# Kernel tuning notes

Hardware: AMD Instinct MI355X
Metric: run time of the kernel (lower is better)

Reference implementation:

```python
import jax, jax.numpy as jnp
import numpy as np

N = 50000      # total nodes across all graphs
E = 1600000    # edges
G = 500        # graphs in batch
F = 128        # input node features
K = 5          # Chebyshev order


def setup_inputs() -> dict:
    key = jax.random.key(0)
    ks = jax.random.split(key, 12)
    x = jax.random.normal(ks[0], (N, F), dtype=jnp.float32)
    edge_index = jax.random.randint(ks[1], (2, E), 0, N)
    edge_attr = jax.random.uniform(ks[2], (E,), dtype=jnp.float32)
    batch = jnp.sort(jax.random.randint(ks[3], (N,), 0, G))
    s = 0.05
    W1 = jax.random.normal(ks[4], (K, F, 64), dtype=jnp.float32) * s
    b1 = jnp.zeros((64,), jnp.float32)
    W2 = jax.random.normal(ks[5], (K, 64, 64), dtype=jnp.float32) * s
    b2 = jnp.zeros((64,), jnp.float32)
    W3 = jax.random.normal(ks[6], (K, 64, 128), dtype=jnp.float32) * s
    b3 = jnp.zeros((128,), jnp.float32)
    Wl = jax.random.normal(ks[7], (128, 2), dtype=jnp.float32) * s
    bl = jnp.zeros((2,), jnp.float32)
    return {"x": x, "edge_index": edge_index, "edge_attr": edge_attr,
            "batch": batch, "W1": W1, "b1": b1, "W2": W2, "b2": b2,
            "W3": W3, "b3": b3, "Wl": Wl, "bl": bl}


def _cheb_conv(x, src, dst, w, Wk, b):
    """PyG ChebConv with lambda_max=2, sym norm: Lhat = -D^-1/2 A D^-1/2
    (the +I diag of L cancels the -I of the rescale, so only off-diag edges).
    Chebyshev recursion: Tx0=x, Tx1=Lhat x, Tx_k = 2 Lhat Tx_{k-1} - Tx_{k-2}."""
    n = x.shape[0]

    def prop(h):  # sparse matvec: out[i] = sum_{e: dst=i} w_e * h[src_e]
        return jax.ops.segment_sum(w[:, None] * h[src], dst, num_segments=n)

    Tx0 = x
    out = Tx0 @ Wk[0]
    Tx1 = prop(Tx0)
    out = out + Tx1 @ Wk[1]
    for k in range(2, Wk.shape[0]):
        Tx2 = 2.0 * prop(Tx1) - Tx0
        out = out + Tx2 @ Wk[k]
        Tx0, Tx1 = Tx1, Tx2
    return out + b


def reference(x, edge_index, edge_attr, batch, W1, b1, W2, b2, W3, b3, Wl, bl):
    src, dst = edge_index[0], edge_index[1]
    # sym-normalized scaled Laplacian edge weights (off-diagonal part)
    deg = jax.ops.segment_sum(edge_attr, src, num_segments=N)
    deg_safe = jnp.where(deg > 0, deg, 1.0)
    dinv = jnp.where(deg > 0, deg_safe ** -0.5, 0.0)
    w = -dinv[src] * edge_attr * dinv[dst]

    h = jax.nn.relu(_cheb_conv(x, src, dst, w, W1, b1))
    # dropout is identity at inference (training=False)
    h = jax.nn.relu(_cheb_conv(h, src, dst, w, W2, b2))
    h = jax.nn.relu(_cheb_conv(h, src, dst, w, W3, b3))

    # global_mean_pool over batch vector
    cnt = jax.ops.segment_sum(jnp.ones((N,), h.dtype), batch, num_segments=G)
    pooled = jax.ops.segment_sum(h, batch, num_segments=G) / jnp.maximum(cnt, 1.0)[:, None]

    logits = pooled @ Wl + bl
    return jax.nn.log_softmax(logits, axis=1)
```

## Files before the change

### kernel.cpp

```cpp
#include <hip/hip_runtime.h>
#include <hip/hip_bf16.h>

#define NN 50000
#define EE 1600000
#define GG 500

#define HB 6250
#define GX1 196
#define GB1 (GX1 * 5)
#define CVB 240

typedef __bf16 bf16x8 __attribute__((ext_vector_type(8)));
typedef float  f32x4  __attribute__((ext_vector_type(4)));

__device__ __forceinline__ float b2f(ushort u) {
  return __uint_as_float(((unsigned)u) << 16);
}
__device__ __forceinline__ ushort f2b(float f) {
  unsigned u = __float_as_uint(f);
  unsigned r = (u + 0x7fff + ((u >> 16) & 1)) >> 16;
  return (ushort)r;
}
__device__ __forceinline__ float lo16(uint v) { return __uint_as_float(v << 16); }
__device__ __forceinline__ float hi16(uint v) { return __uint_as_float(v & 0xffff0000u); }


__global__ __launch_bounds__(256) void mega1(
    const int* __restrict__ src, const int* __restrict__ dst,
    const float* __restrict__ ea, float* __restrict__ deg,
    int* __restrict__ cnt, int* __restrict__ rank,
    const float* __restrict__ x, const float* __restrict__ W1,
    ushort* __restrict__ Acat,
    const float* __restrict__ W2, const float* __restrict__ W3,
    ushort* __restrict__ Wt2, ushort* __restrict__ Wt3)
{
  int b = blockIdx.x;
  if (b < HB) {
    int i = b * 256 + threadIdx.x;
    if (i < EE) {
      atomicAdd(&deg[src[i]], ea[i]);
      rank[i] = atomicAdd(&cnt[dst[i]], 1);
    }
    return;
  }
  b -= HB;
  if (b < GB1) {
    const int bx = b % GX1, by = b / GX1;
    const int lane = threadIdx.x & 63;
    const int wid  = threadIdx.x >> 6;
    const int rb = bx * 256;
    const int cb = by * 64;
    const int lr = lane & 15;
    const int lk = (lane >> 4) << 3;
    f32x4 acc[4][4] = {};
    for (int kc = 0; kc < 128; kc += 64) {
      bf16x8 bfrag[2][4];
      #pragma unroll
      for (int ks = 0; ks < 2; ++ks)
        #pragma unroll
        for (int nt = 0; nt < 4; ++nt) {
          int col = cb + nt * 16 + lr;
          int kk  = kc + ks * 32 + lk;
          const float* wp = &W1[((size_t)(col >> 6) * 128 + kk) * 64 + (col & 63)];
          union { bf16x8 v; ushort u[8]; } bu;
          #pragma unroll
          for (int t = 0; t < 8; ++t) bu.u[t] = f2b(wp[t * 64]);
          bfrag[ks][nt] = bu.v;
        }
      #pragma unroll
      for (int s = 0; s < 4; ++s) {
        const int row = rb + (wid * 4 + s) * 16 + lr;
        #pragma unroll
        for (int ks = 0; ks < 2; ++ks) {
          union { bf16x8 v; ushort u[8]; } au;
          if (row < NN) {
            const float* ap = &x[(size_t)row * 128 + kc + ks * 32 + lk];
            float4 f0 = *(const float4*)ap;
            float4 f1 = *(const float4*)(ap + 4);
            au.u[0] = f2b(f0.x); au.u[1] = f2b(f0.y);
            au.u[2] = f2b(f0.z); au.u[3] = f2b(f0.w);
            au.u[4] = f2b(f1.x); au.u[5] = f2b(f1.y);
            au.u[6] = f2b(f1.z); au.u[7] = f2b(f1.w);
          } else {
            au.v = bf16x8{};
          }
          #pragma unroll
          for (int nt = 0; nt < 4; ++nt)
            acc[s][nt] = __builtin_amdgcn_mfma_f32_16x16x32_bf16(au.v, bfrag[ks][nt],
                                                                 acc[s][nt], 0, 0, 0);
        }
      }
    }
    #pragma unroll
    for (int s = 0; s < 4; ++s)
      #pragma unroll
      for (int nt = 0; nt < 4; ++nt) {
        const int col = cb + nt * 16 + lr;
        #pragma unroll
        for (int r = 0; r < 4; ++r) {
          const int row = rb + (wid * 4 + s) * 16 + ((lane >> 4) << 2) + r;
          if (row < NN) Acat[(size_t)row * 320 + col] = f2b(acc[s][nt][r]);
        }
      }
    return;
  }
  b -= GB1;
  int t = b * 256 + threadIdx.x;
  if (t < 320 * 64) {
    int j = t / 64, k = t % 64;
    Wt2[t] = f2b(W2[((size_t)(j >> 6) * 64 + k) * 64 + (j & 63)]);
  } else {
    int t2 = t - 320 * 64;
    int j = t2 / 320, k = t2 % 320;
    Wt3[t2] = f2b(W3[(size_t)k * 128 + j]);
  }
}


__global__ void scan1(const int* __restrict__ cnt, float* __restrict__ deg,
                      int* __restrict__ partial, int* __restrict__ bsum, int n) {
  __shared__ int s[256];
  int t = threadIdx.x, i = blockIdx.x * 256 + t;
  if (i < n) { float d = deg[i]; deg[i] = (d > 0.f) ? (1.0f / sqrtf(d)) : 0.f; }
  int v = (i < n) ? ((cnt[i] + 7) & ~7) : 0;
  s[t] = v; __syncthreads();
  for (int off = 1; off < 256; off <<= 1) {
    int xv = (t >= off) ? s[t - off] : 0;
    __syncthreads(); s[t] += xv; __syncthreads();
  }
  if (i < n) partial[i] = s[t];
  if (t == 255) bsum[blockIdx.x] = s[255];
}

__global__ void scan2(int* __restrict__ bsum, int nb) {
  __shared__ int s[256];
  int t = threadIdx.x;
  int v = (t < nb) ? bsum[t] : 0;
  s[t] = v; __syncthreads();
  for (int off = 1; off < 256; off <<= 1) {
    int xv = (t >= off) ? s[t - off] : 0;
    __syncthreads(); s[t] += xv; __syncthreads();
  }
  if (t < nb) bsum[t] = s[t];
}

__global__ void scan3(const int* __restrict__ partial, const int* __restrict__ bsum,
                      const int* __restrict__ cnt, int* __restrict__ rowptr,
                      uint2* __restrict__ edges, int n) {
  int i = blockIdx.x * 256 + threadIdx.x;
  if (i < n) {
    int off = (blockIdx.x > 0) ? bsum[blockIdx.x - 1] : 0;
    int end = partial[i] + off;
    rowptr[i + 1] = end;
    if (i == 0) rowptr[0] = 0;
    int c = cnt[i];
    int start = end - ((c + 7) & ~7);
    for (int q = start + c; q < end; ++q) edges[q] = make_uint2(0u, 0u);
  }
}

__global__ void scatter_kernel(const int* __restrict__ src, const int* __restrict__ dst,
                               const float* __restrict__ ea, const float* __restrict__ dinv,
                               const int* __restrict__ rowptr, const int* __restrict__ rank,
                               uint2* __restrict__ edges, int e) {
  int i = blockIdx.x * blockDim.x + threadIdx.x;
  if (i < e) {
    int s = src[i], d = dst[i];
    float w = -dinv[s] * ea[i] * dinv[d];
    edges[rowptr[d] + rank[i]] = make_uint2((unsigned)s, __float_as_uint(w));
  }
}


template<int NADD, bool RELUB>
__global__ __launch_bounds__(256) void prop_kernel(
    const int* __restrict__ rowptr, const uint2* __restrict__ edges,
    const ushort* __restrict__ g, int sg,
    const ushort* __restrict__ a1, int sa1, float c1,
    const ushort* __restrict__ a2, int sa2, float c2,
    const float* __restrict__ bias,
    ushort* __restrict__ out, int so, int n, float alpha)
{
  int wv = blockIdx.x * 4 + (threadIdx.x >> 6);
  wv = __builtin_amdgcn_readfirstlane(wv);
  const int lane = threadIdx.x & 63;
  const int grp = lane >> 3;
  const int sub = lane & 7;
  if (wv >= n) return;
  const int e0 = __builtin_amdgcn_readfirstlane(rowptr[wv]);
  const int e1 = __builtin_amdgcn_readfirstlane(rowptr[wv + 1]);

  float ra[8] = {}, rb[8] = {};
  int j = e0;
  for (; j + 16 <= e1; j += 16) {
    uint2 pa = edges[j + grp];
    uint2 pb = edges[j + 8 + grp];
    uint4 va = *(const uint4*)&g[(size_t)pa.x * sg + sub * 8];
    uint4 vb = *(const uint4*)&g[(size_t)pb.x * sg + sub * 8];
    float wa = __uint_as_float(pa.y);
    float wb = __uint_as_float(pb.y);
    ra[0] += wa * lo16(va.x); ra[1] += wa * hi16(va.x);
    ra[2] += wa * lo16(va.y); ra[3] += wa * hi16(va.y);
    ra[4] += wa * lo16(va.z); ra[5] += wa * hi16(va.z);
    ra[6] += wa * lo16(va.w); ra[7] += wa * hi16(va.w);
    rb[0] += wb * lo16(vb.x); rb[1] += wb * hi16(vb.x);
    rb[2] += wb * lo16(vb.y); rb[3] += wb * hi16(vb.y);
    rb[4] += wb * lo16(vb.z); rb[5] += wb * hi16(vb.z);
    rb[6] += wb * lo16(vb.w); rb[7] += wb * hi16(vb.w);
  }
  if (j < e1) {
    uint2 p = edges[j + grp];
    uint4 v = *(const uint4*)&g[(size_t)p.x * sg + sub * 8];
    float w = __uint_as_float(p.y);
    ra[0] += w * lo16(v.x); ra[1] += w * hi16(v.x);
    ra[2] += w * lo16(v.y); ra[3] += w * hi16(v.y);
    ra[4] += w * lo16(v.z); ra[5] += w * hi16(v.z);
    ra[6] += w * lo16(v.w); ra[7] += w * hi16(v.w);
  }
  float r[8];
  #pragma unroll
  for (int e = 0; e < 8; ++e) {
    float t = ra[e] + rb[e];
    t += __shfl_xor(t, 8, 64);
    t += __shfl_xor(t, 16, 64);
    t += __shfl_xor(t, 32, 64);
    r[e] = alpha * t;
  }
  if constexpr (NADD >= 1) {
    uint4 u = *(const uint4*)&a1[(size_t)wv * sa1 + sub * 8];
    r[0] += c1 * lo16(u.x); r[1] += c1 * hi16(u.x);
    r[2] += c1 * lo16(u.y); r[3] += c1 * hi16(u.y);
    r[4] += c1 * lo16(u.z); r[5] += c1 * hi16(u.z);
    r[6] += c1 * lo16(u.w); r[7] += c1 * hi16(u.w);
  }
  if constexpr (NADD >= 2) {
    uint4 u = *(const uint4*)&a2[(size_t)wv * sa2 + sub * 8];
    r[0] += c2 * lo16(u.x); r[1] += c2 * hi16(u.x);
    r[2] += c2 * lo16(u.y); r[3] += c2 * hi16(u.y);
    r[4] += c2 * lo16(u.z); r[5] += c2 * hi16(u.z);
    r[6] += c2 * lo16(u.w); r[7] += c2 * hi16(u.w);
  }
  if constexpr (RELUB) {
    float4 b0 = *(const float4*)&bias[sub * 8];
    float4 b1 = *(const float4*)&bias[sub * 8 + 4];
    r[0] = fmaxf(r[0] + b0.x, 0.f); r[1] = fmaxf(r[1] + b0.y, 0.f);
    r[2] = fmaxf(r[2] + b0.z, 0.f); r[3] = fmaxf(r[3] + b0.w, 0.f);
    r[4] = fmaxf(r[4] + b1.x, 0.f); r[5] = fmaxf(r[5] + b1.y, 0.f);
    r[6] = fmaxf(r[6] + b1.z, 0.f); r[7] = fmaxf(r[7] + b1.w, 0.f);
  }
  if (grp == 0) {
    uint4 o;
    o.x = (uint)f2b(r[0]) | ((uint)f2b(r[1]) << 16);
    o.y = (uint)f2b(r[2]) | ((uint)f2b(r[3]) << 16);
    o.z = (uint)f2b(r[4]) | ((uint)f2b(r[5]) << 16);
    o.w = (uint)f2b(r[6]) | ((uint)f2b(r[7]) << 16);
    *(uint4*)&out[(size_t)wv * so + sub * 8] = o;
  }
}


template<int Ci, int Co, bool BR>
__global__ __launch_bounds__(256) void gemm_mfma(const ushort* __restrict__ A,
    const ushort* __restrict__ Wt, const float* __restrict__ bias,
    ushort* __restrict__ C, int n)
{
  const int lane = threadIdx.x & 63;
  const int wid  = threadIdx.x >> 6;
  const int rb = blockIdx.x * 256;
  const int cb = blockIdx.y * 64;
  const int lr = lane & 15;
  const int lk = (lane >> 4) << 3;
  f32x4 acc[4][4] = {};

  for (int kc = 0; kc < Ci; kc += 64) {
    bf16x8 bfrag[2][4];
    #pragma unroll
    for (int ks = 0; ks < 2; ++ks)
      #pragma unroll
      for (int nt = 0; nt < 4; ++nt)
        bfrag[ks][nt] = *(const bf16x8*)&Wt[(size_t)(cb + nt * 16 + lr) * Ci + kc + ks * 32 + lk];
    #pragma unroll
    for (int s = 0; s < 4; ++s) {
      const int row = rb + (wid * 4 + s) * 16 + lr;
      const ushort* ap = &A[(size_t)row * Ci + kc + lk];
      #pragma unroll
      for (int ks = 0; ks < 2; ++ks) {
        bf16x8 af = {};
        if (row < n) af = *(const bf16x8*)(ap + ks * 32);
        #pragma unroll
        for (int nt = 0; nt < 4; ++nt)
          acc[s][nt] = __builtin_amdgcn_mfma_f32_16x16x32_bf16(af, bfrag[ks][nt], acc[s][nt], 0, 0, 0);
      }
    }
  }

  #pragma unroll
  for (int s = 0; s < 4; ++s)
    #pragma unroll
    for (int nt = 0; nt < 4; ++nt) {
      const int col = cb + nt * 16 + lr;
      #pragma unroll
      for (int r = 0; r < 4; ++r) {
        const int row = rb + (wid * 4 + s) * 16 + ((lane >> 4) << 2) + r;
        if (row < n) {
          float v = acc[s][nt][r];
          if constexpr (BR) v = fmaxf(v + bias[col], 0.f);
          C[(size_t)row * Co + col] = f2b(v);
        }
      }
    }
}


__global__ __launch_bounds__(128) void pool_kernel(const ushort* __restrict__ h,
    const int* __restrict__ batch, float* __restrict__ pooled,
    float* __restrict__ gcnt, int n) {
  const int f = threadIdx.x;
  const int i0 = blockIdx.x * 64;
  const int iend = min(i0 + 64, n);
  int cur = batch[i0];
  float acc = 0.f;
  int run = 0;
  for (int i = i0; i < iend; ++i) {
    int b = batch[i];
    float v = b2f(h[(size_t)i * 128 + f]);
    if (b != cur) {
      atomicAdd(&pooled[cur * 128 + f], acc);
      if (f == 0) atomicAdd(&gcnt[cur], (float)run);
      acc = 0.f; run = 0; cur = b;
    }
    acc += v; run++;
  }
  atomicAdd(&pooled[cur * 128 + f], acc);
  if (f == 0) atomicAdd(&gcnt[cur], (float)run);
}

__global__ __launch_bounds__(128) void head_kernel(const float* __restrict__ pooled,
    const float* __restrict__ gcnt, const float* __restrict__ Wl,
    const float* __restrict__ bl, float* __restrict__ outp)
{
  int g = blockIdx.x, t = threadIdx.x;
  float denom = fmaxf(gcnt[g], 1.f);
  float p = pooled[g * 128 + t] / denom;
  __shared__ float s0[128], s1[128];
  s0[t] = p * Wl[t * 2 + 0];
  s1[t] = p * Wl[t * 2 + 1];
  __syncthreads();
  for (int off = 64; off > 0; off >>= 1) {
    if (t < off) { s0[t] += s0[t + off]; s1[t] += s1[t + off]; }
    __syncthreads();
  }
  if (t == 0) {
    float a = s0[0] + bl[0], b = s1[0] + bl[1];
    float m = fmaxf(a, b);
    float z = logf(expf(a - m) + expf(b - m)) + m;
    outp[g * 2 + 0] = a - z;
    outp[g * 2 + 1] = b - z;
  }
}


extern "C" void kernel_launch(void* const* d_in, const int* in_sizes, int n_in,
                              void* d_out, int out_size, void* d_ws, size_t ws_size,
                              hipStream_t stream) {
  const float* x   = (const float*)d_in[0];
  const int*   ei  = (const int*)d_in[1];
  const float* ea  = (const float*)d_in[2];
  const int* batch = (const int*)d_in[3];
  const float* W1  = (const float*)d_in[4];
  const float* lb1 = (const float*)d_in[5];
  const float* W2  = (const float*)d_in[6];
  const float* lb2 = (const float*)d_in[7];
  const float* W3  = (const float*)d_in[8];
  const float* lb3 = (const float*)d_in[9];
  const float* Wl  = (const float*)d_in[10];
  const float* bl  = (const float*)d_in[11];
  const int* srcv = ei;
  const int* dstv = ei + EE;

  char* w = (char*)d_ws;
  auto alloc = [&](size_t bytes) -> char* {
    char* p = w; w += (bytes + 255) & ~(size_t)255; return p;
  };
  float* deg    = (float*)alloc((size_t)NN * 4);
  int*   cnt    = (int*)alloc((size_t)NN * 4);
  float* pooled = (float*)alloc((size_t)(GG * 128 + GG) * 4);
  float* gcnt   = pooled + GG * 128;
  char*  zero_end = w;
  int*   rowptr = (int*)alloc((size_t)(NN + 1) * 4);
  int*   bsum   = (int*)alloc(256 * 4);
  int*   rank   = (int*)alloc((size_t)EE * 4);
  uint2* edges  = (uint2*)alloc((size_t)(EE + 8 * NN) * 8);
  ushort* Acat  = (ushort*)alloc((size_t)NN * 320 * 2);
  ushort* Bcat  = (ushort*)alloc((size_t)NN * 320 * 2);
  ushort* h1    = (ushort*)alloc((size_t)NN * 64 * 2);
  ushort* Wt2   = (ushort*)alloc((size_t)320 * 64 * 2);
  ushort* Wt3   = (ushort*)alloc((size_t)128 * 320 * 2);
  int*   partial = (int*)Bcat;
  ushort* h3 = Bcat;

  hipMemsetAsync(deg, 0, (size_t)(zero_end - (char*)deg), stream);

  mega1<<<HB + GB1 + CVB, 256, 0, stream>>>(srcv, dstv, ea, deg, cnt, rank,
                                            x, W1, Acat, W2, W3, Wt2, Wt3);

  const int nb = (NN + 255) / 256;
  scan1<<<nb, 256, 0, stream>>>(cnt, deg, partial, bsum, NN);
  scan2<<<1, 256, 0, stream>>>(bsum, nb);
  scan3<<<nb, 256, 0, stream>>>(partial, bsum, cnt, rowptr, edges, NN);
  scatter_kernel<<<(EE + 255) / 256, 256, 0, stream>>>(srcv, dstv, ea, deg, rowptr, rank,
                                                       edges, EE);

  const int PG = (NN + 3) / 4;
  const int GX = (NN + 255) / 256;

  ushort* A0 = Acat + 0 * 64;  ushort* A1 = Acat + 1 * 64;  ushort* A2 = Acat + 2 * 64;
  ushort* A3 = Acat + 3 * 64;  ushort* A4 = Acat + 4 * 64;
  ushort* B0 = Bcat + 0 * 64;  ushort* B1 = Bcat + 1 * 64;  ushort* B2 = Bcat + 2 * 64;
  ushort* B3 = Bcat + 3 * 64;  ushort* B4 = Bcat + 4 * 64;
  const int S = 320;

  prop_kernel<1, false><<<PG, 256, 0, stream>>>(rowptr, edges, A4, S, A3, S, 1.f,
      nullptr, 0, 0.f, nullptr, A3, S, NN, 2.f);
  prop_kernel<2, false><<<PG, 256, 0, stream>>>(rowptr, edges, A3, S, A2, S, 1.f,
      A4, S, -1.f, nullptr, A2, S, NN, 2.f);
  prop_kernel<2, false><<<PG, 256, 0, stream>>>(rowptr, edges, A2, S, A1, S, 1.f,
      A3, S, -1.f, nullptr, A1, S, NN, 2.f);
  prop_kernel<2, true><<<PG, 256, 0, stream>>>(rowptr, edges, A1, S, A0, S, 1.f,
      A2, S, -1.f, lb1, h1, 64, NN, 1.f);

  gemm_mfma<64, 320, false><<<dim3(GX, 5), 256, 0, stream>>>(h1, Wt2, nullptr, Bcat, NN);
  prop_kernel<1, false><<<PG, 256, 0, stream>>>(rowptr, edges, B4, S, B3, S, 1.f,
      nullptr, 0, 0.f, nullptr, B3, S, NN, 2.f);
  prop_kernel<2, false><<<PG, 256, 0, stream>>>(rowptr, edges, B3, S, B2, S, 1.f,
      B4, S, -1.f, nullptr, B2, S, NN, 2.f);
  prop_kernel<2, false><<<PG, 256, 0, stream>>>(rowptr, edges, B2, S, B1, S, 1.f,
      B3, S, -1.f, nullptr, B1, S, NN, 2.f);
  prop_kernel<2, true><<<PG, 256, 0, stream>>>(rowptr, edges, B1, S, B0, S, 1.f,
      B2, S, -1.f, lb2, A0, S, NN, 1.f);

  prop_kernel<0, false><<<PG, 256, 0, stream>>>(rowptr, edges, A0, S, nullptr, 0, 0.f,
      nullptr, 0, 0.f, nullptr, A1, S, NN, 1.f);
  prop_kernel<1, false><<<PG, 256, 0, stream>>>(rowptr, edges, A1, S, A0, S, -1.f,
      nullptr, 0, 0.f, nullptr, A2, S, NN, 2.f);
  prop_kernel<1, false><<<PG, 256, 0, stream>>>(rowptr, edges, A2, S, A1, S, -1.f,
      nullptr, 0, 0.f, nullptr, A3, S, NN, 2.f);
  prop_kernel<1, false><<<PG, 256, 0, stream>>>(rowptr, edges, A3, S, A2, S, -1.f,
      nullptr, 0, 0.f, nullptr, A4, S, NN, 2.f);
  gemm_mfma<320, 128, true><<<dim3(GX, 2), 256, 0, stream>>>(Acat, Wt3, lb3, h3, NN);

  pool_kernel<<<(NN + 63) / 64, 128, 0, stream>>>(h3, batch, pooled, gcnt, NN);
  head_kernel<<<GG, 128, 0, stream>>>(pooled, gcnt, Wl, bl, (float*)d_out);
}
```

Baseline: 639.8 us.

## Map four nodes per wavefront in sparse propagation and pad rows to four

The sparse propagation kernel now assigns each wavefront four destination nodes, with 16 lanes per node and two edge groups per node, instead of one node per 64-lane wave. CSR row padding drops from multiples of eight to multiples of four, which shrinks the edge buffer and cuts wasted zero-edge work. The cross-lane reduction shrinks to a single shuffle. Average degree is about 32, so the old layout left many lanes idle on partial 16-edge chunks. The trade-offs are per-lane divergence between nodes of unequal degree within a wave, and a grid of NN/16 blocks that assumes NN is divisible by 16 with no bounds check.

```diff
diff --git a/kernel.cpp b/kernel.cpp
--- a/kernel.cpp
+++ b/kernel.cpp
@@ -122,7 +122,7 @@
   __shared__ int s[256];
   int t = threadIdx.x, i = blockIdx.x * 256 + t;
   if (i < n) { float d = deg[i]; deg[i] = (d > 0.f) ? (1.0f / sqrtf(d)) : 0.f; }
-  int v = (i < n) ? ((cnt[i] + 7) & ~7) : 0;
+  int v = (i < n) ? ((cnt[i] + 3) & ~3) : 0;
   s[t] = v; __syncthreads();
   for (int off = 1; off < 256; off <<= 1) {
     int xv = (t >= off) ? s[t - off] : 0;
@@ -154,7 +154,7 @@
     rowptr[i + 1] = end;
     if (i == 0) rowptr[0] = 0;
     int c = cnt[i];
-    int start = end - ((c + 7) & ~7);
+    int start = end - ((c + 3) & ~3);
     for (int q = start + c; q < end; ++q) edges[q] = make_uint2(0u, 0u);
   }
 }
@@ -181,60 +181,49 @@
     const float* __restrict__ bias,
     ushort* __restrict__ out, int so, int n, float alpha)
 {
-  int wv = blockIdx.x * 4 + (threadIdx.x >> 6);
-  wv = __builtin_amdgcn_readfirstlane(wv);
+  const int wave = threadIdx.x >> 6;
   const int lane = threadIdx.x & 63;
-  const int grp = lane >> 3;
-  const int sub = lane & 7;
-  if (wv >= n) return;
-  const int e0 = __builtin_amdgcn_readfirstlane(rowptr[wv]);
-  const int e1 = __builtin_amdgcn_readfirstlane(rowptr[wv + 1]);
+  const int q    = lane >> 4;
+  const int grp  = (lane >> 3) & 1;
+  const int sub  = lane & 7;
+  const int nd = (blockIdx.x * 4 + wave) * 4 + q;
+  const int e0 = rowptr[nd];
+  const int e1 = rowptr[nd + 1];
 
   float ra[8] = {}, rb[8] = {};
-  int j = e0;
-  for (; j + 16 <= e1; j += 16) {
-    uint2 pa = edges[j + grp];
-    uint2 pb = edges[j + 8 + grp];
-    uint4 va = *(const uint4*)&g[(size_t)pa.x * sg + sub * 8];
-    uint4 vb = *(const uint4*)&g[(size_t)pb.x * sg + sub * 8];
-    float wa = __uint_as_float(pa.y);
-    float wb = __uint_as_float(pb.y);
-    ra[0] += wa * lo16(va.x); ra[1] += wa * hi16(va.x);
-    ra[2] += wa * lo16(va.y); ra[3] += wa * hi16(va.y);
-    ra[4] += wa * lo16(va.z); ra[5] += wa * hi16(va.z);
-    ra[6] += wa * lo16(va.w); ra[7] += wa * hi16(va.w);
-    rb[0] += wb * lo16(vb.x); rb[1] += wb * hi16(vb.x);
-    rb[2] += wb * lo16(vb.y); rb[3] += wb * hi16(vb.y);
-    rb[4] += wb * lo16(vb.z); rb[5] += wb * hi16(vb.z);
-    rb[6] += wb * lo16(vb.w); rb[7] += wb * hi16(vb.w);
-  }
-  if (j < e1) {
-    uint2 p = edges[j + grp];
-    uint4 v = *(const uint4*)&g[(size_t)p.x * sg + sub * 8];
-    float w = __uint_as_float(p.y);
-    ra[0] += w * lo16(v.x); ra[1] += w * hi16(v.x);
-    ra[2] += w * lo16(v.y); ra[3] += w * hi16(v.y);
-    ra[4] += w * lo16(v.z); ra[5] += w * hi16(v.z);
-    ra[6] += w * lo16(v.w); ra[7] += w * hi16(v.w);
+  int j = e0 + grp;
+  for (; j + 2 < e1; j += 4) {
+    uint2 p0 = edges[j];
+    uint2 p1 = edges[j + 2];
+    uint4 v0 = *(const uint4*)&g[(size_t)p0.x * sg + sub * 8];
+    uint4 v1 = *(const uint4*)&g[(size_t)p1.x * sg + sub * 8];
+    float w0 = __uint_as_float(p0.y);
+    float w1 = __uint_as_float(p1.y);
+    ra[0] += w0 * lo16(v0.x); ra[1] += w0 * hi16(v0.x);
+    ra[2] += w0 * lo16(v0.y); ra[3] += w0 * hi16(v0.y);
+    ra[4] += w0 * lo16(v0.z); ra[5] += w0 * hi16(v0.z);
+    ra[6] += w0 * lo16(v0.w); ra[7] += w0 * hi16(v0.w);
+    rb[0] += w1 * lo16(v1.x); rb[1] += w1 * hi16(v1.x);
+    rb[2] += w1 * lo16(v1.y); rb[3] += w1 * hi16(v1.y);
+    rb[4] += w1 * lo16(v1.z); rb[5] += w1 * hi16(v1.z);
+    rb[6] += w1 * lo16(v1.w); rb[7] += w1 * hi16(v1.w);
   }
   float r[8];
   #pragma unroll
   for (int e = 0; e < 8; ++e) {
     float t = ra[e] + rb[e];
     t += __shfl_xor(t, 8, 64);
-    t += __shfl_xor(t, 16, 64);
-    t += __shfl_xor(t, 32, 64);
     r[e] = alpha * t;
   }
   if constexpr (NADD >= 1) {
-    uint4 u = *(const uint4*)&a1[(size_t)wv * sa1 + sub * 8];
+    uint4 u = *(const uint4*)&a1[(size_t)nd * sa1 + sub * 8];
     r[0] += c1 * lo16(u.x); r[1] += c1 * hi16(u.x);
     r[2] += c1 * lo16(u.y); r[3] += c1 * hi16(u.y);
     r[4] += c1 * lo16(u.z); r[5] += c1 * hi16(u.z);
     r[6] += c1 * lo16(u.w); r[7] += c1 * hi16(u.w);
   }
   if constexpr (NADD >= 2) {
-    uint4 u = *(const uint4*)&a2[(size_t)wv * sa2 + sub * 8];
+    uint4 u = *(const uint4*)&a2[(size_t)nd * sa2 + sub * 8];
     r[0] += c2 * lo16(u.x); r[1] += c2 * hi16(u.x);
     r[2] += c2 * lo16(u.y); r[3] += c2 * hi16(u.y);
     r[4] += c2 * lo16(u.z); r[5] += c2 * hi16(u.z);
@@ -254,7 +243,7 @@
     o.y = (uint)f2b(r[2]) | ((uint)f2b(r[3]) << 16);
     o.z = (uint)f2b(r[4]) | ((uint)f2b(r[5]) << 16);
     o.w = (uint)f2b(r[6]) | ((uint)f2b(r[7]) << 16);
-    *(uint4*)&out[(size_t)wv * so + sub * 8] = o;
+    *(uint4*)&out[(size_t)nd * so + sub * 8] = o;
   }
 }
 
@@ -390,7 +379,7 @@
   int*   rowptr = (int*)alloc((size_t)(NN + 1) * 4);
   int*   bsum   = (int*)alloc(256 * 4);
   int*   rank   = (int*)alloc((size_t)EE * 4);
-  uint2* edges  = (uint2*)alloc((size_t)(EE + 8 * NN) * 8);
+  uint2* edges  = (uint2*)alloc((size_t)(EE + 4 * NN) * 8);
   ushort* Acat  = (ushort*)alloc((size_t)NN * 320 * 2);
   ushort* Bcat  = (ushort*)alloc((size_t)NN * 320 * 2);
   ushort* h1    = (ushort*)alloc((size_t)NN * 64 * 2);
@@ -411,7 +400,7 @@
   scatter_kernel<<<(EE + 255) / 256, 256, 0, stream>>>(srcv, dstv, ea, deg, rowptr, rank,
                                                        edges, EE);
 
-  const int PG = (NN + 3) / 4;
+  const int PG = NN / 16;
   const int GX = (NN + 255) / 256;
 
   ushort* A0 = Acat + 0 * 64;  ushort* A1 = Acat + 1 * 64;  ushort* A2 = Acat + 2 * 64;
```

Measured after the change: 614.9 us. 1.04x faster.
